# Optimization experiments

Measured on AMD Instinct MI355X. Metric: run time of the kernel, lower is better.

The kernel has to match this reference:

```python
import jax, jax.numpy as jnp
import numpy as np

B, L = 128, 64000
FS, STEP, NFILT, HID, HID2, OUT = 256, 200, 64, 512, 512, 10


def _ilin(lb, ub, W, b=0.0):
    # interval affine: center/radius form
    c = (lb + ub) * 0.5
    r = (ub - lb) * 0.5
    oc = c @ W + b
    orr = r @ jnp.abs(W)
    return oc - orr, oc + orr


def _imul(al, au, bl, bu):
    # interval product: extremes over 4 corner products
    p = jnp.stack([al * bl, al * bu, au * bl, au * bu])
    return p.min(axis=0), p.max(axis=0)


def _cell(xl, xu, hl, hu, cl, cu, wih, whh, bias):
    # interval LSTM cell, torch gate order i,f,g,o
    gl1, gu1 = _ilin(xl, xu, wih)
    gl2, gu2 = _ilin(hl, hu, whh)
    gl = gl1 + gl2 + bias
    gu = gu1 + gu2 + bias
    il, fl, ggl, ol = jnp.split(gl, 4, axis=-1)
    iu, fu, ggu, ou = jnp.split(gu, 4, axis=-1)
    il, iu = jax.nn.sigmoid(il), jax.nn.sigmoid(iu)
    fl, fu = jax.nn.sigmoid(fl), jax.nn.sigmoid(fu)
    ggl, ggu = jnp.tanh(ggl), jnp.tanh(ggu)
    fcl, fcu = _imul(fl, fu, cl, cu)
    igl, igu = _imul(il, iu, ggl, ggu)
    ncl, ncu = fcl + igl, fcu + igu
    nhl, nhu = _imul(jax.nn.sigmoid(ol), jax.nn.sigmoid(ou), jnp.tanh(ncl), jnp.tanh(ncu))
    return nhl, nhu, ncl, ncu


def setup_inputs() -> dict:
    key = jax.random.key(0)
    ks = jax.random.split(key, 13)
    x = 0.1 * jax.random.normal(ks[0], (B, L), jnp.float32)
    eps = 0.01
    s = 0.3  # keep LSTM gates out of saturation
    return {
        "input_lb": x - eps,
        "input_ub": x + eps,
        "mtx1": jax.random.normal(ks[1], (FS, FS + 2), jnp.float32) / np.float32(np.sqrt(FS)),
        "mtx2": jax.random.uniform(ks[2], (FS + 2, NFILT), jnp.float32) / np.float32(FS + 2),
        "lin1_w": jax.random.normal(ks[3], (NFILT, HID), jnp.float32) / np.float32(np.sqrt(NFILT)),
        "lin1_b": 0.01 * jax.random.normal(ks[4], (HID,), jnp.float32),
        "w_ih0": s * jax.random.normal(ks[5], (HID, 4 * HID2), jnp.float32) / np.float32(np.sqrt(HID)),
        "w_hh0": s * jax.random.normal(ks[6], (HID2, 4 * HID2), jnp.float32) / np.float32(np.sqrt(HID2)),
        "b0": 0.01 * jax.random.normal(ks[7], (4 * HID2,), jnp.float32),
        "w_ih1": s * jax.random.normal(ks[8], (HID2, 4 * HID2), jnp.float32) / np.float32(np.sqrt(HID2)),
        "w_hh1": s * jax.random.normal(ks[9], (HID2, 4 * HID2), jnp.float32) / np.float32(np.sqrt(HID2)),
        "b1": 0.01 * jax.random.normal(ks[10], (4 * HID2,), jnp.float32),
        "lin2_w": jax.random.normal(ks[11], (HID2, OUT), jnp.float32) / np.float32(np.sqrt(HID2)),
        "lin2_b": 0.01 * jax.random.normal(ks[12], (OUT,), jnp.float32),
    }


def reference(input_lb, input_ub, mtx1, mtx2, lin1_w, lin1_b,
              w_ih0, w_hh0, b0, w_ih1, w_hh1, b1, lin2_w, lin2_b):
    Bc, Lc = input_lb.shape
    pad = jnp.zeros((Bc, STEP), input_lb.dtype)
    lb = jnp.concatenate([input_lb, pad], axis=1)
    ub = jnp.concatenate([input_ub, pad], axis=1)
    Lp = Lc + STEP
    F = (Lp - FS - 1) // STEP + 1  # frames with i + FS < Lp (break condition)
    idx = jnp.arange(F)[:, None] * STEP + jnp.arange(FS)[None, :]  # [F, FS]
    flb, fub = lb[:, idx], ub[:, idx]  # [B, F, FS]
    # pre-LSTM interval chain, vectorized over all frames
    l1l, l1u = _ilin(flb, fub, mtx1)  # [B, F, FS+2]
    a, b = l1l * l1l, l1u * l1u
    squ = jnp.maximum(a, b)
    sql = jnp.where((l1l <= 0) & (l1u >= 0), 0.0, jnp.minimum(a, b))
    l2l, l2u = _ilin(sql, squ, mtx2, 1e-10)  # mtx2 >= 0, inputs >= 0 -> lb > 0
    lgl, lgu = jnp.log(l2l), jnp.log(l2u)
    n1l, n1u = _ilin(lgl, lgu, lin1_w, lin1_b)  # [B, F, HID]
    rl, ru = jnp.maximum(n1l, 0.0), jnp.maximum(n1u, 0.0)

    H2 = w_hh0.shape[0]
    z = jnp.zeros((Bc, H2), input_lb.dtype)

    def step(carry, xs):
        h0l, h0u, c0l, c0u, h1l, h1u, c1l, c1u = carry
        xl, xu = xs
        h0l, h0u, c0l, c0u = _cell(xl, xu, h0l, h0u, c0l, c0u, w_ih0, w_hh0, b0)
        h1l, h1u, c1l, c1u = _cell(h0l, h0u, h1l, h1u, c1l, c1u, w_ih1, w_hh1, b1)
        return (h0l, h0u, c0l, c0u, h1l, h1u, c1l, c1u), None

    carry, _ = jax.lax.scan(step, (z,) * 8,
                            (jnp.swapaxes(rl, 0, 1), jnp.swapaxes(ru, 0, 1)))
    h1l, h1u = carry[4], carry[5]  # last frame, top LSTM layer
    ol, ou = _ilin(h1l, h1u, lin2_w, lin2_b)
    return jnp.stack([ol, ou])  # [2, B, OUT] logit bounds
```

## Files before the change

### kernel.cpp

```cpp
#include <hip/hip_runtime.h>
#include <hip/hip_bf16.h>
#include <math.h>

#define BATCH 128
#define LEN   64000
#define FS    256
#define STEPS 200
#define NFILT 64
#define HID   512
#define HID2  512
#define NOUT  10
#define NF    320
#define G4    2048
#define KTOT  1024
#define NBLK  256
#define HSLOT (BATCH * HID2)

typedef __bf16  bf16x8 __attribute__((ext_vector_type(8)));
typedef float   f32x4  __attribute__((ext_vector_type(4)));
typedef __hip_bfloat16 hbf;

#define ARV(b)  (128 + (b) * 16)
#define REL_(i) (128 + 4096 + (i) * 16)
#define BAR_WORDS (128 + 4096 + 128)

__device__ __forceinline__ float fsig(float x) { return 1.f / (1.f + __expf(-x)); }
__device__ __forceinline__ float ftanh(float x) { return 1.f - 2.f / (__expf(2.f * x) + 1.f); }
__device__ __forceinline__ void imulf_(float al, float au, float bl, float bu,
                                       float& lo, float& hi) {
    const float p1 = al * bl, p2 = al * bu, p3 = au * bl, p4 = au * bu;
    lo = fminf(fminf(p1, p2), fminf(p3, p4));
    hi = fmaxf(fmaxf(p1, p2), fmaxf(p3, p4));
}

__device__ __forceinline__ bf16x8 loadA16_agent(const hbf* p) {
    union { unsigned long long u[2]; bf16x8 v; } t;
    unsigned long long* q = (unsigned long long*)p;
    t.u[0] = __hip_atomic_load(q,     __ATOMIC_RELAXED, __HIP_MEMORY_SCOPE_AGENT);
    t.u[1] = __hip_atomic_load(q + 1, __ATOMIC_RELAXED, __HIP_MEMORY_SCOPE_AGENT);
    return t.v;
}
__device__ __forceinline__ unsigned ld_flag(const unsigned* p) {
    return __hip_atomic_load(p, __ATOMIC_RELAXED, __HIP_MEMORY_SCOPE_AGENT);
}
__device__ __forceinline__ void st_flag(unsigned* p, unsigned v) {
    __hip_atomic_store(p, v, __ATOMIC_RELAXED, __HIP_MEMORY_SCOPE_AGENT);
}

__global__ __launch_bounds__(512) void frontend_kernel(
    const float* __restrict__ lb, const float* __restrict__ ub,
    const float* __restrict__ mtx1, const float* __restrict__ mtx2,
    const float* __restrict__ lin1_w, const float* __restrict__ lin1_b,
    hbf* __restrict__ Xc, hbf* __restrict__ Xr)
{
    const int tid  = threadIdx.x;
    const int r    = tid >> 6;
    const int lane = tid & 63;
    const int rowid = blockIdx.x * 8 + r;
    const int f = rowid % NF;
    const int b = rowid / NF;

    __shared__ float sc[8][FS], sr[8][FS];
    __shared__ float s2c[8][FS + 2], s2r[8][FS + 2];
    __shared__ float s3c[8][NFILT], s3r[8][NFILT];

    for (int i = lane; i < FS; i += 64) {
        const int pos = f * STEPS + i;
        float l = 0.f, u = 0.f;
        if (pos < LEN) {
            l = lb[(size_t)b * LEN + pos];
            u = ub[(size_t)b * LEN + pos];
        }
        sc[r][i] = 0.5f * (l + u);
        sr[r][i] = 0.5f * (u - l);
    }
    __syncthreads();

    for (int j = lane; j < FS + 2; j += 64) {
        float oc = 0.f, orr = 0.f;
#pragma unroll 4
        for (int i = 0; i < FS; ++i) {
            const float w = mtx1[i * (FS + 2) + j];
            oc  = fmaf(sc[r][i], w, oc);
            orr = fmaf(sr[r][i], fabsf(w), orr);
        }
        const float l1l = oc - orr, l1u = oc + orr;
        const float a = l1l * l1l, bb = l1u * l1u;
        const float squ = fmaxf(a, bb);
        const float sql = (l1l <= 0.f && l1u >= 0.f) ? 0.f : fminf(a, bb);
        s2c[r][j] = 0.5f * (sql + squ);
        s2r[r][j] = 0.5f * (squ - sql);
    }
    __syncthreads();

    {
        const int j = lane;
        float oc = 1e-10f, orr = 0.f;
#pragma unroll 4
        for (int i = 0; i < FS + 2; ++i) {
            const float w = mtx2[i * NFILT + j];
            oc  = fmaf(s2c[r][i], w, oc);
            orr = fmaf(s2r[r][i], fabsf(w), orr);
        }
        const float lgl = logf(oc - orr);
        const float lgu = logf(oc + orr);
        s3c[r][j] = 0.5f * (lgl + lgu);
        s3r[r][j] = 0.5f * (lgu - lgl);
    }
    __syncthreads();

    for (int j = lane; j < HID; j += 64) {
        float oc = lin1_b[j], orr = 0.f;
#pragma unroll 4
        for (int i = 0; i < NFILT; ++i) {
            const float w = lin1_w[i * HID + j];
            oc  = fmaf(s3c[r][i], w, oc);
            orr = fmaf(s3r[r][i], fabsf(w), orr);
        }
        const float n1l = oc - orr, n1u = oc + orr;
        const float rl = fmaxf(n1l, 0.f), ru = fmaxf(n1u, 0.f);
        const size_t o = ((size_t)f * BATCH + b) * HID + j;
        Xc[o] = __float2bfloat16(0.5f * (rl + ru));
        Xr[o] = __float2bfloat16(0.5f * (ru - rl));
    }
}

__global__ __launch_bounds__(256) void prep_weights_kernel(
    const float* __restrict__ wih, const float* __restrict__ whh,
    hbf* __restrict__ Wt)
{
    __shared__ float tile[32][33];
    const int n0 = blockIdx.x * 32;
    const int k0 = blockIdx.y * 32;
    const int tx = threadIdx.x & 31;
    const int ty = threadIdx.x >> 5;

    for (int r = ty; r < 32; r += 8) {
        const int k = k0 + r;
        const float* src = (k < HID) ? (wih + (size_t)k * G4)
                                     : (whh + (size_t)(k - HID) * G4);
        tile[r][tx] = src[n0 + tx];
    }
    __syncthreads();
    for (int r = ty; r < 32; r += 8) {
        const int n = n0 + r;
        Wt[(size_t)n * KTOT + k0 + tx] = __float2bfloat16(tile[tx][r]);
    }
}

__device__ __forceinline__ void gbar(unsigned* bar, unsigned gen,
                                     int bid, int tid) {
    __builtin_amdgcn_s_waitcnt(0);
    __syncthreads();
    if (bid == 0) {
        if (tid != 0) {
            while (ld_flag(&bar[ARV(tid)]) < gen)
                __builtin_amdgcn_s_sleep(1);
        }
        __syncthreads();
        if (tid < 8) st_flag(&bar[REL_(tid)], gen);
    } else {
        if (tid == 0) {
            st_flag(&bar[ARV(bid)], gen);
            while (ld_flag(&bar[REL_(bid & 7)]) < gen)
                __builtin_amdgcn_s_sleep(4);
        }
        asm volatile("" ::: "memory");
    }
    __syncthreads();
}

__device__ __forceinline__ void cell_elem(
    const float C[4], const float R[4], const float bs[4],
    float& cl_r, float& cu_r, float& nhl, float& nhu)
{
    float gl[4], gu[4];
#pragma unroll
    for (int g = 0; g < 4; ++g) {
        gl[g] = C[g] - R[g] + bs[g];
        gu[g] = C[g] + R[g] + bs[g];
    }
    const float il = fsig(gl[0]), iu = fsig(gu[0]);
    const float fl = fsig(gl[1]), fu = fsig(gu[1]);
    const float ggl = ftanh(gl[2]), ggu = ftanh(gu[2]);
    const float ol = fsig(gl[3]), ou = fsig(gu[3]);

    float fcl, fcu, igl, igu;
    imulf_(fl, fu, cl_r, cu_r, fcl, fcu);
    imulf_(il, iu, ggl, ggu, igl, igu);
    const float ncl = fcl + igl, ncu = fcu + igu;
    cl_r = ncl; cu_r = ncu;
    imulf_(ol, ou, ftanh(ncl), ftanh(ncu), nhl, nhu);
}

#define GEMM_HALF(KBASE, MASKED)                                               \
    _Pragma("unroll")                                                          \
    for (int kk = 0; kk < 16; ++kk) {                                          \
        const int KK = (KBASE) + kk;                                           \
        _Pragma("unroll")                                                      \
        for (int g = 0; g < 4; ++g) {                                          \
            union { bf16x8 v; unsigned u[4]; } t2;                             \
            t2.v = *(const bf16x8*)&Wlds[(size_t)(((g << 5) | KK) * 64 + lane) * 8]; \
            if (MASKED) {                                                      \
                t2.u[0] &= 0x7FFF7FFFu; t2.u[1] &= 0x7FFF7FFFu;                \
                t2.u[2] &= 0x7FFF7FFFu; t2.u[3] &= 0x7FFF7FFFu;                \
            }                                                                  \
            acc[g] = __builtin_amdgcn_mfma_f32_16x16x32_bf16(af[kk], t2.v, acc[g], 0, 0, 0); \
        }                                                                      \
    }

#define LOADA16(PTR)                                                           \
    _Pragma("unroll")                                                          \
    for (int i = 0; i < 16; ++i) af[i] = *(const bf16x8*)((PTR) + 32 * i);

#define POLL_GROUP(BASE, TGT)                                                  \
    if (tid < 64) {                                                            \
        const unsigned* pp = &lflags[((BASE) + (tid & 31)) * 16];              \
        for (;;) {                                                             \
            const unsigned v = ld_flag(pp);                                    \
            if (__all((int)v >= (TGT))) break;                                 \
            __builtin_amdgcn_s_sleep(1);                                       \
        }                                                                      \
    }                                                                          \
    __syncthreads();

__global__ __launch_bounds__(256, 1) void lstm_persistent(
    const hbf* Xc, const hbf* Xr,
    hbf* Ring1C, hbf* Ring1R,
    const hbf* __restrict__ Wt0, const hbf* __restrict__ Wt1,
    const float* __restrict__ b0, const float* __restrict__ b1,
    hbf* __restrict__ Ring0C, hbf* __restrict__ Ring0R,
    const hbf* __restrict__ Zbuf,
    hbf* __restrict__ H1c0, hbf* __restrict__ H1r0,
    hbf* __restrict__ H1c1, hbf* __restrict__ H1r1,
    float* __restrict__ h1l, float* __restrict__ h1u,
    unsigned* __restrict__ bar, unsigned* __restrict__ tkt,
    unsigned* __restrict__ lflags)
{
    const int tid = threadIdx.x;
    const int bid = blockIdx.x;

    __shared__ unsigned s_info, s_map;
    __shared__ int s_fast;
    __shared__ hbf   Wlds[4 * 32 * 64 * 8];
    __shared__ float red[2][2][4][64][4];
    __shared__ unsigned short houtC[32][16], houtR[32][16];

    if (tid == 0) {
        unsigned xcc;
        asm volatile("s_getreg_b32 %0, hwreg(HW_REG_XCC_ID)" : "=s"(xcc));
        xcc &= 7u;
        const unsigned slot = __hip_atomic_fetch_add(
            &tkt[xcc * 16], 1u, __ATOMIC_RELAXED, __HIP_MEMORY_SCOPE_AGENT);
        s_info = (xcc << 16) | slot;
    }
    gbar(bar, 1, bid, tid);
    if (tid == 0) {
        unsigned cnt[8]; bool ok = true;
        for (int y = 0; y < 8; ++y) {
            cnt[y] = ld_flag(&tkt[y * 16]);
            ok = ok && (cnt[y] == 32u);
        }
        const unsigned xcc = s_info >> 16, slot = s_info & 0xffffu;
        unsigned rank;
        if (ok) rank = xcc * 32u + slot;
        else { rank = slot; for (unsigned y = 0; y < xcc; ++y) rank += cnt[y]; }
        s_map = rank; s_fast = ok ? 1 : 0;
    }
    __syncthreads();

    const unsigned rank = s_map;
    const bool fast = (s_fast != 0);
    int layer, mgrp, jslot;
    if (fast) { layer = (rank >> 5) & 1; mgrp = rank >> 6; jslot = rank & 31; }
    else      { layer = rank >> 7; mgrp = (rank >> 5) & 3; jslot = rank & 31; }
    const int m0 = mgrp * 32;
    const int j0 = jslot * 16;
    const int lfbase  = layer * 128 + mgrp * 32;
    const int l0fbase = mgrp * 32;
    const int myLf = lfbase + jslot;

    {
        const hbf* Wt = layer ? Wt1 : Wt0;
        for (int c = tid; c < 8192; c += 256) {
            const int g  = c >> 11;
            const int kk = (c >> 6) & 31;
            const int l6 = c & 63;
            const int n  = g * HID2 + j0 + (l6 & 15);
            const int k  = kk * 32 + (l6 >> 4) * 8;
            *(ulonglong2*)&Wlds[(size_t)c * 8] =
                *(const ulonglong2*)(Wt + (size_t)n * KTOT + k);
        }
    }

    const int w    = tid >> 6;
    const int lane = tid & 63;
    const int op   = w & 1;
    const int mh   = w >> 1;
    const int rc   = lane & 15;
    const int gk   = lane >> 4;
    const int aoff = (m0 + mh * 16 + rc) * 512 + 8 * gk;

    hbf* H1cb[2] = { H1c0, H1c1 };
    hbf* H1rb[2] = { H1r0, H1r1 };

    const int mm  = tid >> 4;
    const int cj  = tid & 15;
    const int ll  = ((mm >> 2) << 4) | cj;
    const int rr  = mm & 3;
    const int idx0 = (m0 + mm) * HID2 + j0 + cj;
    const int idx1 = idx0 + 16 * HID2;
    const float* bias = layer ? b1 : b0;
    float bs[4];
#pragma unroll
    for (int g = 0; g < 4; ++g) bs[g] = bias[g * HID2 + j0 + cj];

    const int st_arr = tid >> 7;
    const int st_row = (tid >> 2) & 31;
    const int st_q   = tid & 3;
    const size_t st_off = (size_t)(m0 + st_row) * 512 + j0 + st_q * 4;

    float cAl = 0.f, cAu = 0.f, cBl = 0.f, cBu = 0.f;

    __syncthreads();

    for (int t = 0; t < NF; ++t) {
        const int wslot = t & 1, rslot = wslot ^ 1;
        f32x4 acc[4] = {f32x4{0,0,0,0}, f32x4{0,0,0,0},
                        f32x4{0,0,0,0}, f32x4{0,0,0,0}};
        bf16x8 af[16];

        if (layer == 0) {
            {
                const hbf* p = (op ? Xr : Xc) + (size_t)t * HSLOT + aoff;
                LOADA16(p)
                if (op) { GEMM_HALF(0, 1) } else { GEMM_HALF(0, 0) }
            }
            POLL_GROUP(lfbase, t)
            {
                const int pt = (t == 0) ? NF : t - 1;
                const hbf* p = (op ? Ring0R : Ring0C) + (size_t)pt * HSLOT + aoff;
                LOADA16(p)
                if (op) { GEMM_HALF(16, 1) } else { GEMM_HALF(16, 0) }
            }
        } else {
            POLL_GROUP(lfbase, t)
            if (fast) {
                const hbf* p = (t == 0) ? (Zbuf + aoff)
                    : ((op ? (const hbf*)Ring1R : (const hbf*)Ring1C)
                       + (size_t)(t - 1) * HSLOT + aoff);
                LOADA16(p)
            } else {
                const hbf* p = (op ? H1rb[rslot] : H1cb[rslot]) + aoff;
#pragma unroll
                for (int i = 0; i < 16; ++i) af[i] = loadA16_agent(p + 32 * i);
            }
            if (op) { GEMM_HALF(16, 1) } else { GEMM_HALF(16, 0) }
            POLL_GROUP(l0fbase, t + 1)
            {
                const hbf* p = (op ? Ring0R : Ring0C) + (size_t)t * HSLOT + aoff;
                LOADA16(p)
                if (op) { GEMM_HALF(0, 1) } else { GEMM_HALF(0, 0) }
            }
        }

#pragma unroll
        for (int g = 0; g < 4; ++g)
            *((f32x4*)&red[op][mh][g][lane][0]) = acc[g];
        __syncthreads();

        {
            float C0[4], R0[4], C1[4], R1[4];
#pragma unroll
            for (int g = 0; g < 4; ++g) {
                C0[g] = red[0][0][g][ll][rr];
                R0[g] = red[1][0][g][ll][rr];
                C1[g] = red[0][1][g][ll][rr];
                R1[g] = red[1][1][g][ll][rr];
            }
            const bool writeF = (layer == 1) && (t == NF - 1);

            float nhl, nhu;
            cell_elem(C0, R0, bs, cAl, cAu, nhl, nhu);
            {
                const __hip_bfloat16 hc = __float2bfloat16(0.5f * (nhl + nhu));
                const __hip_bfloat16 hr = __float2bfloat16(0.5f * (nhu - nhl));
                houtC[mm][cj] = *(const unsigned short*)&hc;
                houtR[mm][cj] = *(const unsigned short*)&hr;
            }
            if (writeF) { h1l[idx0] = nhl; h1u[idx0] = nhu; }

            cell_elem(C1, R1, bs, cBl, cBu, nhl, nhu);
            {
                const __hip_bfloat16 hc = __float2bfloat16(0.5f * (nhl + nhu));
                const __hip_bfloat16 hr = __float2bfloat16(0.5f * (nhu - nhl));
                houtC[mm + 16][cj] = *(const unsigned short*)&hc;
                houtR[mm + 16][cj] = *(const unsigned short*)&hr;
            }
            if (writeF) { h1l[idx1] = nhl; h1u[idx1] = nhu; }
        }
        __syncthreads();

        {
            hbf *dstC, *dstR;
            if (layer == 0) {
                dstC = Ring0C + (size_t)t * HSLOT;
                dstR = Ring0R + (size_t)t * HSLOT;
            } else if (fast) {
                dstC = Ring1C + (size_t)t * HSLOT;
                dstR = Ring1R + (size_t)t * HSLOT;
            } else {
                dstC = H1cb[wslot];
                dstR = H1rb[wslot];
            }
            const unsigned long long* src = (const unsigned long long*)
                &(st_arr ? houtR : houtC)[st_row][st_q * 4];
            unsigned long long* dst = (unsigned long long*)
                ((st_arr ? dstR : dstC) + st_off);
            __hip_atomic_store(dst, *src, __ATOMIC_RELAXED,
                               __HIP_MEMORY_SCOPE_AGENT);
        }

        __builtin_amdgcn_s_waitcnt(0);
        __syncthreads();
        if (tid == 0)
            st_flag(&lflags[myLf * 16], (unsigned)(t + 1));
    }
}

__global__ __launch_bounds__(64) void final_kernel(
    const float* __restrict__ h1l, const float* __restrict__ h1u,
    const float* __restrict__ w, const float* __restrict__ bias,
    float* __restrict__ out)
{
    const int b = blockIdx.x;
    const int j = threadIdx.x;
    if (j < NOUT) {
        float oc = bias[j], orr = 0.f;
        for (int i = 0; i < HID2; ++i) {
            const float lo = h1l[(size_t)b * HID2 + i];
            const float hi = h1u[(size_t)b * HID2 + i];
            const float wv = w[i * NOUT + j];
            oc  = fmaf(0.5f * (lo + hi), wv, oc);
            orr = fmaf(0.5f * (hi - lo), fabsf(wv), orr);
        }
        out[b * NOUT + j] = oc - orr;
        out[BATCH * NOUT + b * NOUT + j] = oc + orr;
    }
}

extern "C" void kernel_launch(void* const* d_in, const int* in_sizes, int n_in,
                              void* d_out, int out_size, void* d_ws, size_t ws_size,
                              hipStream_t stream)
{
    const float* input_lb = (const float*)d_in[0];
    const float* input_ub = (const float*)d_in[1];
    const float* mtx1     = (const float*)d_in[2];
    const float* mtx2     = (const float*)d_in[3];
    const float* lin1_w   = (const float*)d_in[4];
    const float* lin1_b   = (const float*)d_in[5];
    const float* w_ih0    = (const float*)d_in[6];
    const float* w_hh0    = (const float*)d_in[7];
    const float* b0       = (const float*)d_in[8];
    const float* w_ih1    = (const float*)d_in[9];
    const float* w_hh1    = (const float*)d_in[10];
    const float* b1       = (const float*)d_in[11];
    const float* lin2_w   = (const float*)d_in[12];
    const float* lin2_b   = (const float*)d_in[13];
    float* out = (float*)d_out;

    char* ws = (char*)d_ws;
    size_t off = 0;
    hbf* Xc = (hbf*)(ws + off); off += (size_t)NF * HSLOT * 2;
    hbf* Xr = (hbf*)(ws + off); off += (size_t)NF * HSLOT * 2;
    hbf* Wt0 = (hbf*)(ws + off); off += (size_t)G4 * KTOT * 2;
    hbf* Wt1 = (hbf*)(ws + off); off += (size_t)G4 * KTOT * 2;
    hbf* Ring0C = (hbf*)(ws + off); off += (size_t)(NF + 1) * HSLOT * 2;
    hbf* Ring0R = (hbf*)(ws + off); off += (size_t)(NF + 1) * HSLOT * 2;

    char* zbase = ws + off;
    hbf* Zbuf = (hbf*)(ws + off); off += (size_t)HSLOT * 2;
    hbf* H1c0 = (hbf*)(ws + off); off += (size_t)HSLOT * 2;
    hbf* H1r0 = (hbf*)(ws + off); off += (size_t)HSLOT * 2;
    hbf* H1c1 = (hbf*)(ws + off); off += (size_t)HSLOT * 2;
    hbf* H1r1 = (hbf*)(ws + off); off += (size_t)HSLOT * 2;
    unsigned* lflags = (unsigned*)(ws + off); off += (size_t)256 * 16 * 4;
    unsigned* tkt    = (unsigned*)(ws + off); off += (size_t)8 * 16 * 4;
    unsigned* bar    = (unsigned*)(ws + off); off += (size_t)BAR_WORDS * 4;
    const size_t zbytes = (size_t)((ws + off) - zbase);
    float* h1l = (float*)(ws + off); off += (size_t)HSLOT * 4;
    float* h1u = (float*)(ws + off); off += (size_t)HSLOT * 4;

    hipMemsetAsync(zbase, 0, zbytes, stream);
    hipMemsetAsync(Ring0C + (size_t)NF * HSLOT, 0, (size_t)HSLOT * 2, stream);
    hipMemsetAsync(Ring0R + (size_t)NF * HSLOT, 0, (size_t)HSLOT * 2, stream);

    {
        const dim3 pgrid(G4 / 32, KTOT / 32);
        prep_weights_kernel<<<pgrid, 256, 0, stream>>>(w_ih0, w_hh0, Wt0);
        prep_weights_kernel<<<pgrid, 256, 0, stream>>>(w_ih1, w_hh1, Wt1);
    }

    frontend_kernel<<<(BATCH * NF) / 8, 512, 0, stream>>>(
        input_lb, input_ub, mtx1, mtx2, lin1_w, lin1_b, Xc, Xr);

    lstm_persistent<<<NBLK, 256, 0, stream>>>(
        Xc, Xr, Xc, Xr, Wt0, Wt1, b0, b1,
        Ring0C, Ring0R, Zbuf,
        H1c0, H1r0, H1c1, H1r1,
        h1l, h1u, bar, tkt, lflags);

    final_kernel<<<BATCH, 64, 0, stream>>>(h1l, h1u, lin2_w, lin2_b, out);
}
```

Measured before the change: 3.399 ms.

## Use bf16 MFMA for frontend mtx1 matmul and prefetch layer-0 input tiles

The frontend's first interval matmul (256x258) moves from scalar fp32 FMAs to bf16 MFMA. mtx1 is pre-transposed into a padded bf16 matrix, and the abs of the weights is taken for the radius path by masking the sign bit. Each block now handles 16 frames and stages its tiles in shared memory. Separately, the layer-0 LSTM loop prefetches the next step's input tile into registers while the current GEMM runs, to hide load latency on the recurrent critical path. In exchange, the first matmul loses precision (bf16 instead of fp32 inputs) and register pressure rises in the persistent kernel.

Measured after the change: 3.448 ms. About the same (+1.4%).

```diff
diff --git a/kernel.cpp b/kernel.cpp
--- a/kernel.cpp
+++ b/kernel.cpp
@@ -47,104 +47,168 @@
     __hip_atomic_store(p, v, __ATOMIC_RELAXED, __HIP_MEMORY_SCOPE_AGENT);
 }
 
-__global__ __launch_bounds__(512) void frontend_kernel(
+__global__ __launch_bounds__(256) void prep_weights_kernel(
+    const float* __restrict__ wih, const float* __restrict__ whh,
+    hbf* __restrict__ Wt)
+{
+    __shared__ float tile[32][33];
+    const int n0 = blockIdx.x * 32;
+    const int k0 = blockIdx.y * 32;
+    const int tx = threadIdx.x & 31;
+    const int ty = threadIdx.x >> 5;
+
+    for (int r = ty; r < 32; r += 8) {
+        const int k = k0 + r;
+        const float* src = (k < HID) ? (wih + (size_t)k * G4)
+                                     : (whh + (size_t)(k - HID) * G4);
+        tile[r][tx] = src[n0 + tx];
+    }
+    __syncthreads();
+    for (int r = ty; r < 32; r += 8) {
+        const int n = n0 + r;
+        Wt[(size_t)n * KTOT + k0 + tx] = __float2bfloat16(tile[tx][r]);
+    }
+}
+
+__global__ __launch_bounds__(256) void prep_mtx1_kernel(
+    const float* __restrict__ mtx1, hbf* __restrict__ W)
+{
+    __shared__ float tile[32][33];
+    const int n0 = blockIdx.x * 32;
+    const int k0 = blockIdx.y * 32;
+    const int tx = threadIdx.x & 31;
+    const int ty = threadIdx.x >> 5;
+
+    for (int r = ty; r < 32; r += 8) {
+        const int k = k0 + r;
+        const int n = n0 + tx;
+        tile[r][tx] = (n < FS + 2) ? mtx1[k * (FS + 2) + n] : 0.f;
+    }
+    __syncthreads();
+    for (int r = ty; r < 32; r += 8) {
+        const int n = n0 + r;
+        if (n < 272)
+            W[(size_t)n * 256 + k0 + tx] = __float2bfloat16(tile[tx][r]);
+    }
+}
+
+#define FB_A1   0
+#define FB_OUT1 35840
+#define FB_S2   0
+#define FB_S3   35840
+#define FB_SIZE 70656
+
+__global__ __launch_bounds__(256) void frontend2_kernel(
     const float* __restrict__ lb, const float* __restrict__ ub,
-    const float* __restrict__ mtx1, const float* __restrict__ mtx2,
+    const hbf* __restrict__ Wt1f,
+    const float* __restrict__ mtx2,
     const float* __restrict__ lin1_w, const float* __restrict__ lin1_b,
     hbf* __restrict__ Xc, hbf* __restrict__ Xr)
 {
-    const int tid  = threadIdx.x;
-    const int r    = tid >> 6;
-    const int lane = tid & 63;
-    const int rowid = blockIdx.x * 8 + r;
-    const int f = rowid % NF;
-    const int b = rowid / NF;
-
-    __shared__ float sc[8][FS], sr[8][FS];
-    __shared__ float s2c[8][FS + 2], s2r[8][FS + 2];
-    __shared__ float s3c[8][NFILT], s3r[8][NFILT];
-
-    for (int i = lane; i < FS; i += 64) {
+    __shared__ char fbuf[FB_SIZE];
+    hbf*   A1c = (hbf*)(fbuf + FB_A1);
+    hbf*   A1r = (hbf*)(fbuf + FB_A1 + 16 * 264 * 2);
+    float* o1C = (float*)(fbuf + FB_OUT1);
+    float* o1R = (float*)(fbuf + FB_OUT1 + 16 * 272 * 4);
+    float* s2c = (float*)(fbuf + FB_S2);
+    float* s2r = (float*)(fbuf + FB_S2 + 16 * 258 * 4);
+    float* s3c = (float*)(fbuf + FB_S3);
+    float* s3r = (float*)(fbuf + FB_S3 + 16 * 64 * 4);
+
+    const int tid = threadIdx.x;
+    const int row0 = blockIdx.x * 16;
+
+    for (int c = tid; c < 16 * 256; c += 256) {
+        const int m = c >> 8, i = c & 255;
+        const int rowid = row0 + m;
+        const int f = rowid % NF, b = rowid / NF;
         const int pos = f * STEPS + i;
         float l = 0.f, u = 0.f;
         if (pos < LEN) {
             l = lb[(size_t)b * LEN + pos];
             u = ub[(size_t)b * LEN + pos];
         }
-        sc[r][i] = 0.5f * (l + u);
-        sr[r][i] = 0.5f * (u - l);
-    }
-    __syncthreads();
-
-    for (int j = lane; j < FS + 2; j += 64) {
-        float oc = 0.f, orr = 0.f;
-#pragma unroll 4
-        for (int i = 0; i < FS; ++i) {
-            const float w = mtx1[i * (FS + 2) + j];
-            oc  = fmaf(sc[r][i], w, oc);
-            orr = fmaf(sr[r][i], fabsf(w), orr);
-        }
+        A1c[m * 264 + i] = __float2bfloat16(0.5f * (l + u));
+        A1r[m * 264 + i] = __float2bfloat16(0.5f * (u - l));
+    }
+    __syncthreads();
+
+    {
+        const int w    = tid >> 6;
+        const int lane = tid & 63;
+        const int op   = w & 1;
+        const int nh   = w >> 1;
+        const int rc   = lane & 15;
+        const int gk   = lane >> 4;
+        const unsigned amask = op ? 0x7FFF7FFFu : 0xFFFFFFFFu;
+        const hbf* ap = (op ? A1r : A1c) + rc * 264 + 8 * gk;
+        float* outp = op ? o1R : o1C;
+
+        for (int nt = nh * 9; nt < nh * 8 + 9; ++nt) {
+            f32x4 acc = {0.f, 0.f, 0.f, 0.f};
+            const hbf* bp = Wt1f + (size_t)(nt * 16 + rc) * 256 + 8 * gk;
+#pragma unroll
+            for (int k0 = 0; k0 < 256; k0 += 32) {
+                const bf16x8 afr = *(const bf16x8*)(ap + k0);
+                union { bf16x8 v; unsigned u[4]; } t2;
+                t2.v = *(const bf16x8*)(bp + k0);
+                t2.u[0] &= amask; t2.u[1] &= amask;
+                t2.u[2] &= amask; t2.u[3] &= amask;
+                acc = __builtin_amdgcn_mfma_f32_16x16x32_bf16(afr, t2.v, acc, 0, 0, 0);
+            }
+            const int n = nt * 16 + rc;
+#pragma unroll
+            for (int reg = 0; reg < 4; ++reg)
+                outp[(4 * gk + reg) * 272 + n] = acc[reg];
+        }
+    }
+    __syncthreads();
+
+    for (int c = tid; c < 16 * 258; c += 256) {
+        const int m = c / 258, n = c - m * 258;
+        const float oc = o1C[m * 272 + n];
+        const float orr = o1R[m * 272 + n];
         const float l1l = oc - orr, l1u = oc + orr;
         const float a = l1l * l1l, bb = l1u * l1u;
         const float squ = fmaxf(a, bb);
         const float sql = (l1l <= 0.f && l1u >= 0.f) ? 0.f : fminf(a, bb);
-        s2c[r][j] = 0.5f * (sql + squ);
-        s2r[r][j] = 0.5f * (squ - sql);
-    }
-    __syncthreads();
-
-    {
-        const int j = lane;
+        s2c[m * 258 + n] = 0.5f * (sql + squ);
+        s2r[m * 258 + n] = 0.5f * (squ - sql);
+    }
+    __syncthreads();
+
+    for (int idx = tid; idx < 16 * 64; idx += 256) {
+        const int m = idx >> 6, n = idx & 63;
         float oc = 1e-10f, orr = 0.f;
 #pragma unroll 4
         for (int i = 0; i < FS + 2; ++i) {
-            const float w = mtx2[i * NFILT + j];
-            oc  = fmaf(s2c[r][i], w, oc);
-            orr = fmaf(s2r[r][i], fabsf(w), orr);
+            const float w = mtx2[i * NFILT + n];
+            oc  = fmaf(s2c[m * 258 + i], w, oc);
+            orr = fmaf(s2r[m * 258 + i], fabsf(w), orr);
         }
         const float lgl = logf(oc - orr);
         const float lgu = logf(oc + orr);
-        s3c[r][j] = 0.5f * (lgl + lgu);
-        s3r[r][j] = 0.5f * (lgu - lgl);
-    }
-    __syncthreads();
-
-    for (int j = lane; j < HID; j += 64) {
+        s3c[m * 64 + n] = 0.5f * (lgl + lgu);
+        s3r[m * 64 + n] = 0.5f * (lgu - lgl);
+    }
+    __syncthreads();
+
+    for (int idx = tid; idx < 16 * 512; idx += 256) {
+        const int m = idx >> 9, j = idx & 511;
         float oc = lin1_b[j], orr = 0.f;
 #pragma unroll 4
         for (int i = 0; i < NFILT; ++i) {
             const float w = lin1_w[i * HID + j];
-            oc  = fmaf(s3c[r][i], w, oc);
-            orr = fmaf(s3r[r][i], fabsf(w), orr);
+            oc  = fmaf(s3c[m * 64 + i], w, oc);
+            orr = fmaf(s3r[m * 64 + i], fabsf(w), orr);
         }
         const float n1l = oc - orr, n1u = oc + orr;
         const float rl = fmaxf(n1l, 0.f), ru = fmaxf(n1u, 0.f);
+        const int rowid = row0 + m;
+        const int f = rowid % NF, b = rowid / NF;
         const size_t o = ((size_t)f * BATCH + b) * HID + j;
         Xc[o] = __float2bfloat16(0.5f * (rl + ru));
         Xr[o] = __float2bfloat16(0.5f * (ru - rl));
-    }
-}
-
-__global__ __launch_bounds__(256) void prep_weights_kernel(
-    const float* __restrict__ wih, const float* __restrict__ whh,
-    hbf* __restrict__ Wt)
-{
-    __shared__ float tile[32][33];
-    const int n0 = blockIdx.x * 32;
-    const int k0 = blockIdx.y * 32;
-    const int tx = threadIdx.x & 31;
-    const int ty = threadIdx.x >> 5;
-
-    for (int r = ty; r < 32; r += 8) {
-        const int k = k0 + r;
-        const float* src = (k < HID) ? (wih + (size_t)k * G4)
-                                     : (whh + (size_t)(k - HID) * G4);
-        tile[r][tx] = src[n0 + tx];
-    }
-    __syncthreads();
-    for (int r = ty; r < 32; r += 8) {
-        const int n = n0 + r;
-        Wt[(size_t)n * KTOT + k0 + tx] = __float2bfloat16(tile[tx][r]);
     }
 }
 
@@ -324,41 +388,54 @@
 
     __syncthreads();
 
+    bf16x8 xf[16];
+    if (layer == 0) {
+        const hbf* p = (op ? Xr : Xc) + aoff;
+        bf16x8* af = xf;
+        LOADA16(p)
+    }
+
     for (int t = 0; t < NF; ++t) {
         const int wslot = t & 1, rslot = wslot ^ 1;
         f32x4 acc[4] = {f32x4{0,0,0,0}, f32x4{0,0,0,0},
                         f32x4{0,0,0,0}, f32x4{0,0,0,0}};
-        bf16x8 af[16];
 
         if (layer == 0) {
             {
-                const hbf* p = (op ? Xr : Xc) + (size_t)t * HSLOT + aoff;
+                bf16x8* af = xf;
+                if (op) { GEMM_HALF(0, 1) } else { GEMM_HALF(0, 0) }
+                const int tn = (t + 1 < NF) ? (t + 1) : t;
+                const hbf* p = (op ? Xr : Xc) + (size_t)tn * HSLOT + aoff;
                 LOADA16(p)
-                if (op) { GEMM_HALF(0, 1) } else { GEMM_HALF(0, 0) }
             }
             POLL_GROUP(lfbase, t)
             {
                 const int pt = (t == 0) ? NF : t - 1;
                 const hbf* p = (op ? Ring0R : Ring0C) + (size_t)pt * HSLOT + aoff;
+                bf16x8 af[16];
                 LOADA16(p)
                 if (op) { GEMM_HALF(16, 1) } else { GEMM_HALF(16, 0) }
             }
         } else {
             POLL_GROUP(lfbase, t)
-            if (fast) {
-                const hbf* p = (t == 0) ? (Zbuf + aoff)
-                    : ((op ? (const hbf*)Ring1R : (const hbf*)Ring1C)
-                       + (size_t)(t - 1) * HSLOT + aoff);
-                LOADA16(p)
-            } else {
-                const hbf* p = (op ? H1rb[rslot] : H1cb[rslot]) + aoff;
-#pragma unroll
-                for (int i = 0; i < 16; ++i) af[i] = loadA16_agent(p + 32 * i);
-            }
-            if (op) { GEMM_HALF(16, 1) } else { GEMM_HALF(16, 0) }
+            {
+                bf16x8 af[16];
+                if (fast) {
+                    const hbf* p = (t == 0) ? (Zbuf + aoff)
+                        : ((op ? (const hbf*)Ring1R : (const hbf*)Ring1C)
+                           + (size_t)(t - 1) * HSLOT + aoff);
+                    LOADA16(p)
+                } else {
+                    const hbf* p = (op ? H1rb[rslot] : H1cb[rslot]) + aoff;
+#pragma unroll
+                    for (int i = 0; i < 16; ++i) af[i] = loadA16_agent(p + 32 * i);
+                }
+                if (op) { GEMM_HALF(16, 1) } else { GEMM_HALF(16, 0) }
+            }
             POLL_GROUP(l0fbase, t + 1)
             {
                 const hbf* p = (op ? Ring0R : Ring0C) + (size_t)t * HSLOT + aoff;
+                bf16x8 af[16];
                 LOADA16(p)
                 if (op) { GEMM_HALF(0, 1) } else { GEMM_HALF(0, 0) }
             }
@@ -475,6 +552,7 @@
     hbf* Xr = (hbf*)(ws + off); off += (size_t)NF * HSLOT * 2;
     hbf* Wt0 = (hbf*)(ws + off); off += (size_t)G4 * KTOT * 2;
     hbf* Wt1 = (hbf*)(ws + off); off += (size_t)G4 * KTOT * 2;
+    hbf* Wt1f = (hbf*)(ws + off); off += (size_t)272 * 256 * 2;
     hbf* Ring0C = (hbf*)(ws + off); off += (size_t)(NF + 1) * HSLOT * 2;
     hbf* Ring0R = (hbf*)(ws + off); off += (size_t)(NF + 1) * HSLOT * 2;
 
@@ -499,10 +577,11 @@
         const dim3 pgrid(G4 / 32, KTOT / 32);
         prep_weights_kernel<<<pgrid, 256, 0, stream>>>(w_ih0, w_hh0, Wt0);
         prep_weights_kernel<<<pgrid, 256, 0, stream>>>(w_ih1, w_hh1, Wt1);
-    }
-
-    frontend_kernel<<<(BATCH * NF) / 8, 512, 0, stream>>>(
-        input_lb, input_ub, mtx1, mtx2, lin1_w, lin1_b, Xc, Xr);
+        prep_mtx1_kernel<<<dim3(9, 8), 256, 0, stream>>>(mtx1, Wt1f);
+    }
+
+    frontend2_kernel<<<(BATCH * NF) / 16, 256, 0, stream>>>(
+        input_lb, input_ub, Wt1f, mtx2, lin1_w, lin1_b, Xc, Xr);
 
     lstm_persistent<<<NBLK, 256, 0, stream>>>(
         Xc, Xr, Xc, Xr, Wt0, Wt1, b0, b1,
```
